# Kernel tuning notes

Hardware: AMD Instinct MI355X
Metric: run time of the kernel (lower is better)

## Reference

```python
import jax, jax.numpy as jnp
import numpy as np

KAPPA = 20.0
STAGES = 10
NUM_PRO = 3
EPS = 1e-6


def _l2norm(x, axis):
    return x / (EPS + jnp.linalg.norm(x, axis=axis, keepdims=True))


def _em(x, mu):
    # x: [b, c, n]; mu: [b, c, k]
    def step(mu, _):
        z = jax.nn.softmax(KAPPA * jnp.einsum('bcn,bck->bnk', x, mu), axis=2)  # [b,n,k]
        z_ = z / (EPS + z.sum(axis=1, keepdims=True))
        mu = _l2norm(jnp.einsum('bcn,bnk->bck', x, z_), axis=1)
        return mu, None
    mu, _ = jax.lax.scan(step, mu, None, length=STAGES)
    return jnp.transpose(mu, (0, 2, 1))  # [b, k, c]


def setup_inputs() -> dict:
    key = jax.random.key(0)
    k1, k2, k3, k4 = jax.random.split(key, 4)
    b, c, h, w, k = 16, 512, 64, 64, NUM_PRO
    support_feature = jax.random.normal(k1, (b, c, h, w), dtype=jnp.float32)
    support_mask = jax.random.uniform(k2, (b, 1, h, w), dtype=jnp.float32)
    query_feature = jax.random.normal(k3, (b, c, h, w), dtype=jnp.float32)
    mu = jax.random.normal(k4, (1, c, k), dtype=jnp.float32) * np.sqrt(2.0 / k)
    return {"support_feature": support_feature, "support_mask": support_mask,
            "query_feature": query_feature, "mu": mu}


def reference(support_feature, support_mask, query_feature, mu):
    b, c, h, w = support_feature.shape
    n = h * w
    mu0 = jnp.broadcast_to(_l2norm(mu, axis=1), (b, c, NUM_PRO))
    # mask already at feature resolution -> bilinear align_corners resize is identity
    z_fg = (support_mask * support_feature).reshape(b, c, n)
    z_bg = ((1.0 - support_mask) * support_feature).reshape(b, c, n)
    mu_f = _em(z_fg, mu0)  # [b, k, c]
    mu_b = _em(z_bg, mu0)  # [b, k, c]
    # discriminative model on query
    mu_cat = jnp.concatenate([mu_f, mu_b], axis=1)  # [b, 2k, c]
    xq = query_feature.reshape(b, c, n)
    z = jax.nn.softmax(jnp.einsum('bcn,bkc->bnk', xq, mu_cat), axis=2)  # [b, n, 2k]
    P = jnp.transpose(z, (0, 2, 1)).reshape(b, 2 * NUM_PRO, h, w)
    P_f = P[:, :NUM_PRO].sum(axis=1, keepdims=True)
    P_b = P[:, NUM_PRO:].sum(axis=1, keepdims=True)
    Prob_map = jnp.concatenate([P_b, P_f], axis=1)  # [b, 2, h, w]
    return (mu_f, mu_b, Prob_map, P)
```

## Files before the change

kernel.cpp:

```cpp
#include <hip/hip_runtime.h>
#include <cstdint>
#include <cstddef>

#define EPS 1e-6f
#define KAPPA 20.0f

#define B 16
#define C 512
#define N 4096
#define J 6
#define XS_STRIDE 513

__global__ __launch_bounds__(512) void pmms_init(const float* __restrict__ mu_in,
                                                 float* __restrict__ mu_cur,
                                                 float* __restrict__ mu_acc) {
  int b = blockIdx.x;
  int c = threadIdx.x;
  float v0 = mu_in[c * 3 + 0], v1 = mu_in[c * 3 + 1], v2 = mu_in[c * 3 + 2];
  float s0 = v0 * v0, s1 = v1 * v1, s2 = v2 * v2;
  for (int o = 32; o; o >>= 1) {
    s0 += __shfl_down(s0, o);
    s1 += __shfl_down(s1, o);
    s2 += __shfl_down(s2, o);
  }
  __shared__ float r[8][3];
  int w = c >> 6, ln = c & 63;
  if (ln == 0) { r[w][0] = s0; r[w][1] = s1; r[w][2] = s2; }
  __syncthreads();
  float t0 = 0.f, t1 = 0.f, t2 = 0.f;
  for (int i = 0; i < 8; ++i) { t0 += r[i][0]; t1 += r[i][1]; t2 += r[i][2]; }
  float sc0 = 1.0f / (EPS + sqrtf(t0));
  float sc1 = 1.0f / (EPS + sqrtf(t1));
  float sc2 = 1.0f / (EPS + sqrtf(t2));
  float n0 = v0 * sc0, n1 = v1 * sc1, n2 = v2 * sc2;
  size_t base = ((size_t)b * C + c) * J;
  mu_cur[base + 0] = n0; mu_cur[base + 1] = n1; mu_cur[base + 2] = n2;
  mu_cur[base + 3] = n0; mu_cur[base + 4] = n1; mu_cur[base + 5] = n2;
  #pragma unroll
  for (int j = 0; j < J; ++j) mu_acc[base + j] = 0.0f;
}

__global__ __launch_bounds__(256, 1) void pmms_stage(const float* __restrict__ feat,
                                                     const float* __restrict__ mask,
                                                     const float* __restrict__ mu_cur,
                                                     float* __restrict__ mu_acc) {
  extern __shared__ float s[];
  float* xs  = s;
  float* mus = xs + 64 * XS_STRIDE;
  float* ms  = mus + C * 8;
  float* zs  = ms + 64;
  float* ps  = zs + 64 * 8;

  int b  = blockIdx.x >> 4;
  int wg = blockIdx.x & 15;
  int tid = threadIdx.x;

  for (int i = tid; i < C * J; i += 256) {
    int c = i / 6, j = i - c * 6;
    mus[c * 8 + j] = mu_cur[(size_t)b * C * J + i];
  }

  float acc[12];
  #pragma unroll
  for (int j = 0; j < 12; ++j) acc[j] = 0.0f;

  const int wv = tid >> 6, ln = tid & 63;

  for (int t = 0; t < 4; ++t) {
    int n0 = (wg * 4 + t) * 64;
    __syncthreads();
    {
      int rpt = tid >> 4, seg = tid & 15;
      const float* fb = feat + (size_t)b * C * N + n0;
      for (int cb = 0; cb < C; cb += 16) {
        int c = cb + rpt;
        float4 v = *(const float4*)(fb + (size_t)c * N + seg * 4);
        int nl = seg * 4;
        xs[(nl + 0) * XS_STRIDE + c] = v.x;
        xs[(nl + 1) * XS_STRIDE + c] = v.y;
        xs[(nl + 2) * XS_STRIDE + c] = v.z;
        xs[(nl + 3) * XS_STRIDE + c] = v.w;
      }
      if (tid < 16) {
        float4 v = *(const float4*)(mask + (size_t)b * N + n0 + tid * 4);
        ms[tid * 4 + 0] = v.x; ms[tid * 4 + 1] = v.y;
        ms[tid * 4 + 2] = v.z; ms[tid * 4 + 3] = v.w;
      }
    }
    __syncthreads();
    {
      float m = ms[ln];
      float lf0 = 0.f, lf1 = 0.f, lf2 = 0.f, lb0 = 0.f, lb1 = 0.f, lb2 = 0.f;
      int cbeg = wv * 128;
      #pragma unroll 4
      for (int c = cbeg; c < cbeg + 128; ++c) {
        float f = xs[ln * XS_STRIDE + c];
        float xf = m * f, xb = f - xf;
        float4 m03 = *(const float4*)(mus + c * 8);
        float2 m45 = *(const float2*)(mus + c * 8 + 4);
        lf0 = fmaf(xf, m03.x, lf0); lf1 = fmaf(xf, m03.y, lf1); lf2 = fmaf(xf, m03.z, lf2);
        lb0 = fmaf(xb, m03.w, lb0); lb1 = fmaf(xb, m45.x, lb1); lb2 = fmaf(xb, m45.y, lb2);
      }
      float* pr = ps + (wv * 64 + ln) * 8;
      pr[0] = lf0; pr[1] = lf1; pr[2] = lf2; pr[3] = lb0; pr[4] = lb1; pr[5] = lb2;
    }
    __syncthreads();
    if (tid < 64) {
      float L[6];
      #pragma unroll
      for (int j = 0; j < 6; ++j)
        L[j] = ps[(0 * 64 + tid) * 8 + j] + ps[(1 * 64 + tid) * 8 + j] +
               ps[(2 * 64 + tid) * 8 + j] + ps[(3 * 64 + tid) * 8 + j];
      float mf = fmaxf(fmaxf(L[0], L[1]), L[2]);
      float e0 = __expf(KAPPA * (L[0] - mf));
      float e1 = __expf(KAPPA * (L[1] - mf));
      float e2 = __expf(KAPPA * (L[2] - mf));
      float is = 1.0f / (e0 + e1 + e2);
      zs[tid * 8 + 0] = e0 * is; zs[tid * 8 + 1] = e1 * is; zs[tid * 8 + 2] = e2 * is;
      float mb = fmaxf(fmaxf(L[3], L[4]), L[5]);
      e0 = __expf(KAPPA * (L[3] - mb));
      e1 = __expf(KAPPA * (L[4] - mb));
      e2 = __expf(KAPPA * (L[5] - mb));
      is = 1.0f / (e0 + e1 + e2);
      zs[tid * 8 + 3] = e0 * is; zs[tid * 8 + 4] = e1 * is; zs[tid * 8 + 5] = e2 * is;
    }
    __syncthreads();
    {
      int c0 = tid, c1 = tid + 256;
      #pragma unroll 4
      for (int n = 0; n < 64; ++n) {
        float m2 = ms[n];
        float4 z03 = *(const float4*)(zs + n * 8);
        float2 z45 = *(const float2*)(zs + n * 8 + 4);
        float f0 = xs[n * XS_STRIDE + c0];
        float xf = m2 * f0, xb = f0 - xf;
        acc[0] = fmaf(xf, z03.x, acc[0]); acc[1] = fmaf(xf, z03.y, acc[1]); acc[2] = fmaf(xf, z03.z, acc[2]);
        acc[3] = fmaf(xb, z03.w, acc[3]); acc[4] = fmaf(xb, z45.x, acc[4]); acc[5] = fmaf(xb, z45.y, acc[5]);
        float f1 = xs[n * XS_STRIDE + c1];
        xf = m2 * f1; xb = f1 - xf;
        acc[6] = fmaf(xf, z03.x, acc[6]); acc[7]  = fmaf(xf, z03.y, acc[7]);  acc[8]  = fmaf(xf, z03.z, acc[8]);
        acc[9] = fmaf(xb, z03.w, acc[9]); acc[10] = fmaf(xb, z45.x, acc[10]); acc[11] = fmaf(xb, z45.y, acc[11]);
      }
    }
  }
  float* dst = mu_acc + (size_t)b * C * J;
  #pragma unroll
  for (int j = 0; j < 6; ++j) atomicAdd(dst + tid * 6 + j, acc[j]);
  #pragma unroll
  for (int j = 0; j < 6; ++j) atomicAdd(dst + (size_t)(tid + 256) * 6 + j, acc[6 + j]);
}

__global__ __launch_bounds__(256) void pmms_norm(float* __restrict__ mu_acc,
                                                 float* __restrict__ mu_cur,
                                                 float* __restrict__ out_f,
                                                 float* __restrict__ out_b,
                                                 int write_out) {
  int b = blockIdx.x / 6, j = blockIdx.x % 6;
  int tid = threadIdx.x;
  size_t base = (size_t)b * C * J + j;
  float v0 = mu_acc[base + (size_t)tid * 6];
  float v1 = mu_acc[base + (size_t)(tid + 256) * 6];
  float ss = v0 * v0 + v1 * v1;
  for (int o = 32; o; o >>= 1) ss += __shfl_down(ss, o);
  __shared__ float r[4];
  if ((tid & 63) == 0) r[tid >> 6] = ss;
  __syncthreads();
  float tot = r[0] + r[1] + r[2] + r[3];
  float sc = 1.0f / (EPS + sqrtf(tot));
  float n0 = v0 * sc, n1 = v1 * sc;
  mu_cur[base + (size_t)tid * 6] = n0;
  mu_cur[base + (size_t)(tid + 256) * 6] = n1;
  mu_acc[base + (size_t)tid * 6] = 0.0f;
  mu_acc[base + (size_t)(tid + 256) * 6] = 0.0f;
  if (write_out) {
    float* o = (j < 3) ? (out_f + (size_t)b * 1536 + j * 512)
                       : (out_b + (size_t)b * 1536 + (j - 3) * 512);
    o[tid] = n0;
    o[tid + 256] = n1;
  }
}

__global__ __launch_bounds__(256) void pmms_query(const float* __restrict__ q,
                                                  const float* __restrict__ mu_cur,
                                                  float* __restrict__ P,
                                                  float* __restrict__ PM) {
  __shared__ float mus[C * 8];
  int b = blockIdx.x >> 4;
  int n = ((blockIdx.x & 15) << 8) + threadIdx.x;
  for (int i = threadIdx.x; i < C * J; i += 256) {
    int c = i / 6, j = i - c * 6;
    mus[c * 8 + j] = mu_cur[(size_t)b * C * J + i];
  }
  __syncthreads();
  float l0 = 0.f, l1 = 0.f, l2 = 0.f, l3 = 0.f, l4 = 0.f, l5 = 0.f;
  const float* qb = q + (size_t)b * C * N + n;
  #pragma unroll 4
  for (int c = 0; c < C; ++c) {
    float xv = qb[(size_t)c * N];
    float4 m03 = *(const float4*)(mus + c * 8);
    float2 m45 = *(const float2*)(mus + c * 8 + 4);
    l0 = fmaf(xv, m03.x, l0); l1 = fmaf(xv, m03.y, l1); l2 = fmaf(xv, m03.z, l2);
    l3 = fmaf(xv, m03.w, l3); l4 = fmaf(xv, m45.x, l4); l5 = fmaf(xv, m45.y, l5);
  }
  float mx = fmaxf(fmaxf(fmaxf(l0, l1), fmaxf(l2, l3)), fmaxf(l4, l5));
  float e0 = __expf(l0 - mx), e1 = __expf(l1 - mx), e2 = __expf(l2 - mx);
  float e3 = __expf(l3 - mx), e4 = __expf(l4 - mx), e5 = __expf(l5 - mx);
  float is = 1.0f / (e0 + e1 + e2 + e3 + e4 + e5);
  float z0 = e0 * is, z1 = e1 * is, z2 = e2 * is;
  float z3 = e3 * is, z4 = e4 * is, z5 = e5 * is;
  float* Pb = P + (size_t)b * 6 * N;
  Pb[0 * N + n] = z0; Pb[1 * N + n] = z1; Pb[2 * N + n] = z2;
  Pb[3 * N + n] = z3; Pb[4 * N + n] = z4; Pb[5 * N + n] = z5;
  float* pm = PM + (size_t)b * 2 * N;
  pm[n] = z3 + z4 + z5;
  pm[N + n] = z0 + z1 + z2;
}

extern "C" void kernel_launch(void* const* d_in, const int* in_sizes, int n_in,
                              void* d_out, int out_size, void* d_ws, size_t ws_size,
                              hipStream_t stream) {
  const float* feat  = (const float*)d_in[0];
  const float* mask  = (const float*)d_in[1];
  const float* query = (const float*)d_in[2];
  const float* mu_in = (const float*)d_in[3];
  float* out = (float*)d_out;

  float* mu_cur = (float*)d_ws;
  float* mu_acc = mu_cur + (size_t)B * C * J;

  const int smem = (64 * XS_STRIDE + C * 8 + 64 + 64 * 8 + 4 * 64 * 8) * 4;
  (void)hipFuncSetAttribute((const void*)pmms_stage,
                            hipFuncAttributeMaxDynamicSharedMemorySize, smem);

  pmms_init<<<B, 512, 0, stream>>>(mu_in, mu_cur, mu_acc);
  for (int st = 0; st < 10; ++st) {
    pmms_stage<<<256, 256, smem, stream>>>(feat, mask, mu_cur, mu_acc);
    pmms_norm<<<96, 256, 0, stream>>>(mu_acc, mu_cur, out, out + 24576, st == 9 ? 1 : 0);
  }
  pmms_query<<<256, 256, 0, stream>>>(query, mu_cur, out + 180224, out + 49152);
}
```

Baseline: 943.2 us.

## Drop shared-memory feature transpose; stream features twice from global with smaller tiles

The stage kernel no longer stages a 64x512 transposed feature tile in LDS. It computes logits straight from global float4 loads, using 8-lane channel splits reduced with shuffles. The weighted sum then rereads the same 128-column tile from global, hoping for L2 hits. Cutting LDS use from about 150KB to about 19KB lets up to 6 blocks share a CU, and the grid grows to 512 blocks. The query kernel uses the same vectorised, shuffle-reduced layout with float4 output stores. The risk is that every stage now reads the features from global twice.

Measured after the change: 1.431 ms. 1.52x slower.

```diff
diff --git a/kernel.cpp b/kernel.cpp
--- a/kernel.cpp
+++ b/kernel.cpp
@@ -9,7 +9,8 @@
 #define C 512
 #define N 4096
 #define J 6
-#define XS_STRIDE 513
+#define NT 128
+#define NTILES (N / NT)
 
 __global__ __launch_bounds__(512) void pmms_init(const float* __restrict__ mu_in,
                                                  float* __restrict__ mu_cur,
@@ -40,106 +41,128 @@
   for (int j = 0; j < J; ++j) mu_acc[base + j] = 0.0f;
 }
 
-__global__ __launch_bounds__(256, 1) void pmms_stage(const float* __restrict__ feat,
+__global__ __launch_bounds__(256, 6) void pmms_stage(const float* __restrict__ feat,
                                                      const float* __restrict__ mask,
                                                      const float* __restrict__ mu_cur,
                                                      float* __restrict__ mu_acc) {
-  extern __shared__ float s[];
-  float* xs  = s;
-  float* mus = xs + 64 * XS_STRIDE;
-  float* ms  = mus + C * 8;
-  float* zs  = ms + 64;
-  float* ps  = zs + 64 * 8;
-
-  int b  = blockIdx.x >> 4;
-  int wg = blockIdx.x & 15;
-  int tid = threadIdx.x;
+  __shared__ float mus[C * 8];
+  __shared__ float zs[J][NT];
+  __shared__ float ms[NT];
+
+  const int b  = blockIdx.x >> 5;
+  const int n0 = (blockIdx.x & 31) * NT;
+  const int tid = threadIdx.x;
 
   for (int i = tid; i < C * J; i += 256) {
     int c = i / 6, j = i - c * 6;
     mus[c * 8 + j] = mu_cur[(size_t)b * C * J + i];
   }
+  if (tid < NT / 4) {
+    *(float4*)(ms + tid * 4) = *(const float4*)(mask + (size_t)b * N + n0 + tid * 4);
+  }
+  __syncthreads();
+
+  {
+    const int cc = tid & 7, ng = tid >> 3;
+    const int nb = n0 + ng * 4;
+    float4 m4 = *(const float4*)(ms + ng * 4);
+    float L[J][4];
+    #pragma unroll
+    for (int j = 0; j < J; ++j)
+      #pragma unroll
+      for (int k = 0; k < 4; ++k) L[j][k] = 0.0f;
+    const float* fb = feat + (size_t)b * C * N + nb;
+    #pragma unroll 4
+    for (int i = 0; i < C / 8; ++i) {
+      int c = cc + i * 8;
+      float4 f   = *(const float4*)(fb + (size_t)c * N);
+      float4 m03 = *(const float4*)(mus + c * 8);
+      float2 m45 = *(const float2*)(mus + c * 8 + 4);
+      float fa[4] = {f.x, f.y, f.z, f.w};
+      float ma[4] = {m4.x, m4.y, m4.z, m4.w};
+      #pragma unroll
+      for (int k = 0; k < 4; ++k) {
+        float xf = ma[k] * fa[k];
+        float xb = fa[k] - xf;
+        L[0][k] = fmaf(xf, m03.x, L[0][k]);
+        L[1][k] = fmaf(xf, m03.y, L[1][k]);
+        L[2][k] = fmaf(xf, m03.z, L[2][k]);
+        L[3][k] = fmaf(xb, m03.w, L[3][k]);
+        L[4][k] = fmaf(xb, m45.x, L[4][k]);
+        L[5][k] = fmaf(xb, m45.y, L[5][k]);
+      }
+    }
+    #pragma unroll
+    for (int d = 1; d < 8; d <<= 1)
+      #pragma unroll
+      for (int j = 0; j < J; ++j)
+        #pragma unroll
+        for (int k = 0; k < 4; ++k)
+          L[j][k] += __shfl_xor(L[j][k], d);
+    float zv[J][4];
+    #pragma unroll
+    for (int k = 0; k < 4; ++k) {
+      float mf = fmaxf(fmaxf(L[0][k], L[1][k]), L[2][k]);
+      float e0 = __expf(KAPPA * (L[0][k] - mf));
+      float e1 = __expf(KAPPA * (L[1][k] - mf));
+      float e2 = __expf(KAPPA * (L[2][k] - mf));
+      float is = 1.0f / (e0 + e1 + e2);
+      zv[0][k] = e0 * is; zv[1][k] = e1 * is; zv[2][k] = e2 * is;
+      float mb = fmaxf(fmaxf(L[3][k], L[4][k]), L[5][k]);
+      e0 = __expf(KAPPA * (L[3][k] - mb));
+      e1 = __expf(KAPPA * (L[4][k] - mb));
+      e2 = __expf(KAPPA * (L[5][k] - mb));
+      is = 1.0f / (e0 + e1 + e2);
+      zv[3][k] = e0 * is; zv[4][k] = e1 * is; zv[5][k] = e2 * is;
+    }
+    if (cc == 0) {
+      int nl = ng * 4;
+      #pragma unroll
+      for (int j = 0; j < J; ++j)
+        *(float4*)(&zs[j][nl]) = make_float4(zv[j][0], zv[j][1], zv[j][2], zv[j][3]);
+    }
+  }
+  __syncthreads();
 
   float acc[12];
   #pragma unroll
   for (int j = 0; j < 12; ++j) acc[j] = 0.0f;
-
-  const int wv = tid >> 6, ln = tid & 63;
-
-  for (int t = 0; t < 4; ++t) {
-    int n0 = (wg * 4 + t) * 64;
-    __syncthreads();
-    {
-      int rpt = tid >> 4, seg = tid & 15;
-      const float* fb = feat + (size_t)b * C * N + n0;
-      for (int cb = 0; cb < C; cb += 16) {
-        int c = cb + rpt;
-        float4 v = *(const float4*)(fb + (size_t)c * N + seg * 4);
-        int nl = seg * 4;
-        xs[(nl + 0) * XS_STRIDE + c] = v.x;
-        xs[(nl + 1) * XS_STRIDE + c] = v.y;
-        xs[(nl + 2) * XS_STRIDE + c] = v.z;
-        xs[(nl + 3) * XS_STRIDE + c] = v.w;
-      }
-      if (tid < 16) {
-        float4 v = *(const float4*)(mask + (size_t)b * N + n0 + tid * 4);
-        ms[tid * 4 + 0] = v.x; ms[tid * 4 + 1] = v.y;
-        ms[tid * 4 + 2] = v.z; ms[tid * 4 + 3] = v.w;
-      }
-    }
-    __syncthreads();
-    {
-      float m = ms[ln];
-      float lf0 = 0.f, lf1 = 0.f, lf2 = 0.f, lb0 = 0.f, lb1 = 0.f, lb2 = 0.f;
-      int cbeg = wv * 128;
-      #pragma unroll 4
-      for (int c = cbeg; c < cbeg + 128; ++c) {
-        float f = xs[ln * XS_STRIDE + c];
-        float xf = m * f, xb = f - xf;
-        float4 m03 = *(const float4*)(mus + c * 8);
-        float2 m45 = *(const float2*)(mus + c * 8 + 4);
-        lf0 = fmaf(xf, m03.x, lf0); lf1 = fmaf(xf, m03.y, lf1); lf2 = fmaf(xf, m03.z, lf2);
-        lb0 = fmaf(xb, m03.w, lb0); lb1 = fmaf(xb, m45.x, lb1); lb2 = fmaf(xb, m45.y, lb2);
-      }
-      float* pr = ps + (wv * 64 + ln) * 8;
-      pr[0] = lf0; pr[1] = lf1; pr[2] = lf2; pr[3] = lb0; pr[4] = lb1; pr[5] = lb2;
-    }
-    __syncthreads();
-    if (tid < 64) {
-      float L[6];
-      #pragma unroll
-      for (int j = 0; j < 6; ++j)
-        L[j] = ps[(0 * 64 + tid) * 8 + j] + ps[(1 * 64 + tid) * 8 + j] +
-               ps[(2 * 64 + tid) * 8 + j] + ps[(3 * 64 + tid) * 8 + j];
-      float mf = fmaxf(fmaxf(L[0], L[1]), L[2]);
-      float e0 = __expf(KAPPA * (L[0] - mf));
-      float e1 = __expf(KAPPA * (L[1] - mf));
-      float e2 = __expf(KAPPA * (L[2] - mf));
-      float is = 1.0f / (e0 + e1 + e2);
-      zs[tid * 8 + 0] = e0 * is; zs[tid * 8 + 1] = e1 * is; zs[tid * 8 + 2] = e2 * is;
-      float mb = fmaxf(fmaxf(L[3], L[4]), L[5]);
-      e0 = __expf(KAPPA * (L[3] - mb));
-      e1 = __expf(KAPPA * (L[4] - mb));
-      e2 = __expf(KAPPA * (L[5] - mb));
-      is = 1.0f / (e0 + e1 + e2);
-      zs[tid * 8 + 3] = e0 * is; zs[tid * 8 + 4] = e1 * is; zs[tid * 8 + 5] = e2 * is;
-    }
-    __syncthreads();
-    {
-      int c0 = tid, c1 = tid + 256;
-      #pragma unroll 4
-      for (int n = 0; n < 64; ++n) {
-        float m2 = ms[n];
-        float4 z03 = *(const float4*)(zs + n * 8);
-        float2 z45 = *(const float2*)(zs + n * 8 + 4);
-        float f0 = xs[n * XS_STRIDE + c0];
-        float xf = m2 * f0, xb = f0 - xf;
-        acc[0] = fmaf(xf, z03.x, acc[0]); acc[1] = fmaf(xf, z03.y, acc[1]); acc[2] = fmaf(xf, z03.z, acc[2]);
-        acc[3] = fmaf(xb, z03.w, acc[3]); acc[4] = fmaf(xb, z45.x, acc[4]); acc[5] = fmaf(xb, z45.y, acc[5]);
-        float f1 = xs[n * XS_STRIDE + c1];
-        xf = m2 * f1; xb = f1 - xf;
-        acc[6] = fmaf(xf, z03.x, acc[6]); acc[7]  = fmaf(xf, z03.y, acc[7]);  acc[8]  = fmaf(xf, z03.z, acc[8]);
-        acc[9] = fmaf(xb, z03.w, acc[9]); acc[10] = fmaf(xb, z45.x, acc[10]); acc[11] = fmaf(xb, z45.y, acc[11]);
+  {
+    const int c0 = tid, c1 = tid + 256;
+    const float* f0p = feat + ((size_t)b * C + c0) * N + n0;
+    const float* f1p = feat + ((size_t)b * C + c1) * N + n0;
+    #pragma unroll 2
+    for (int g = 0; g < NT / 4; ++g) {
+      float4 f0 = *(const float4*)(f0p + g * 4);
+      float4 f1 = *(const float4*)(f1p + g * 4);
+      float4 mm = *(const float4*)(ms + g * 4);
+      float4 z0 = *(const float4*)(&zs[0][g * 4]);
+      float4 z1 = *(const float4*)(&zs[1][g * 4]);
+      float4 z2 = *(const float4*)(&zs[2][g * 4]);
+      float4 z3 = *(const float4*)(&zs[3][g * 4]);
+      float4 z4 = *(const float4*)(&zs[4][g * 4]);
+      float4 z5 = *(const float4*)(&zs[5][g * 4]);
+      float fa0[4] = {f0.x, f0.y, f0.z, f0.w};
+      float fa1[4] = {f1.x, f1.y, f1.z, f1.w};
+      float mk[4]  = {mm.x, mm.y, mm.z, mm.w};
+      float za[J][4] = {{z0.x,z0.y,z0.z,z0.w},{z1.x,z1.y,z1.z,z1.w},{z2.x,z2.y,z2.z,z2.w},
+                        {z3.x,z3.y,z3.z,z3.w},{z4.x,z4.y,z4.z,z4.w},{z5.x,z5.y,z5.z,z5.w}};
+      #pragma unroll
+      for (int k = 0; k < 4; ++k) {
+        float xf = mk[k] * fa0[k], xb = fa0[k] - xf;
+        acc[0] = fmaf(xf, za[0][k], acc[0]);
+        acc[1] = fmaf(xf, za[1][k], acc[1]);
+        acc[2] = fmaf(xf, za[2][k], acc[2]);
+        acc[3] = fmaf(xb, za[3][k], acc[3]);
+        acc[4] = fmaf(xb, za[4][k], acc[4]);
+        acc[5] = fmaf(xb, za[5][k], acc[5]);
+        xf = mk[k] * fa1[k]; xb = fa1[k] - xf;
+        acc[6]  = fmaf(xf, za[0][k], acc[6]);
+        acc[7]  = fmaf(xf, za[1][k], acc[7]);
+        acc[8]  = fmaf(xf, za[2][k], acc[8]);
+        acc[9]  = fmaf(xb, za[3][k], acc[9]);
+        acc[10] = fmaf(xb, za[4][k], acc[10]);
+        acc[11] = fmaf(xb, za[5][k], acc[11]);
       }
     }
   }
@@ -180,40 +203,76 @@
   }
 }
 
-__global__ __launch_bounds__(256) void pmms_query(const float* __restrict__ q,
-                                                  const float* __restrict__ mu_cur,
-                                                  float* __restrict__ P,
-                                                  float* __restrict__ PM) {
+__global__ __launch_bounds__(256, 6) void pmms_query(const float* __restrict__ q,
+                                                     const float* __restrict__ mu_cur,
+                                                     float* __restrict__ P,
+                                                     float* __restrict__ PM) {
   __shared__ float mus[C * 8];
-  int b = blockIdx.x >> 4;
-  int n = ((blockIdx.x & 15) << 8) + threadIdx.x;
-  for (int i = threadIdx.x; i < C * J; i += 256) {
+  const int b  = blockIdx.x >> 5;
+  const int n0 = (blockIdx.x & 31) * NT;
+  const int tid = threadIdx.x;
+  for (int i = tid; i < C * J; i += 256) {
     int c = i / 6, j = i - c * 6;
     mus[c * 8 + j] = mu_cur[(size_t)b * C * J + i];
   }
   __syncthreads();
-  float l0 = 0.f, l1 = 0.f, l2 = 0.f, l3 = 0.f, l4 = 0.f, l5 = 0.f;
-  const float* qb = q + (size_t)b * C * N + n;
+  const int cc = tid & 7, ng = tid >> 3;
+  const int nb = n0 + ng * 4;
+  float L[J][4];
+  #pragma unroll
+  for (int j = 0; j < J; ++j)
+    #pragma unroll
+    for (int k = 0; k < 4; ++k) L[j][k] = 0.0f;
+  const float* qb = q + (size_t)b * C * N + nb;
   #pragma unroll 4
-  for (int c = 0; c < C; ++c) {
-    float xv = qb[(size_t)c * N];
+  for (int i = 0; i < C / 8; ++i) {
+    int c = cc + i * 8;
+    float4 f   = *(const float4*)(qb + (size_t)c * N);
     float4 m03 = *(const float4*)(mus + c * 8);
     float2 m45 = *(const float2*)(mus + c * 8 + 4);
-    l0 = fmaf(xv, m03.x, l0); l1 = fmaf(xv, m03.y, l1); l2 = fmaf(xv, m03.z, l2);
-    l3 = fmaf(xv, m03.w, l3); l4 = fmaf(xv, m45.x, l4); l5 = fmaf(xv, m45.y, l5);
-  }
-  float mx = fmaxf(fmaxf(fmaxf(l0, l1), fmaxf(l2, l3)), fmaxf(l4, l5));
-  float e0 = __expf(l0 - mx), e1 = __expf(l1 - mx), e2 = __expf(l2 - mx);
-  float e3 = __expf(l3 - mx), e4 = __expf(l4 - mx), e5 = __expf(l5 - mx);
-  float is = 1.0f / (e0 + e1 + e2 + e3 + e4 + e5);
-  float z0 = e0 * is, z1 = e1 * is, z2 = e2 * is;
-  float z3 = e3 * is, z4 = e4 * is, z5 = e5 * is;
-  float* Pb = P + (size_t)b * 6 * N;
-  Pb[0 * N + n] = z0; Pb[1 * N + n] = z1; Pb[2 * N + n] = z2;
-  Pb[3 * N + n] = z3; Pb[4 * N + n] = z4; Pb[5 * N + n] = z5;
-  float* pm = PM + (size_t)b * 2 * N;
-  pm[n] = z3 + z4 + z5;
-  pm[N + n] = z0 + z1 + z2;
+    float fa[4] = {f.x, f.y, f.z, f.w};
+    #pragma unroll
+    for (int k = 0; k < 4; ++k) {
+      L[0][k] = fmaf(fa[k], m03.x, L[0][k]);
+      L[1][k] = fmaf(fa[k], m03.y, L[1][k]);
+      L[2][k] = fmaf(fa[k], m03.z, L[2][k]);
+      L[3][k] = fmaf(fa[k], m03.w, L[3][k]);
+      L[4][k] = fmaf(fa[k], m45.x, L[4][k]);
+      L[5][k] = fmaf(fa[k], m45.y, L[5][k]);
+    }
+  }
+  #pragma unroll
+  for (int d = 1; d < 8; d <<= 1)
+    #pragma unroll
+    for (int j = 0; j < J; ++j)
+      #pragma unroll
+      for (int k = 0; k < 4; ++k)
+        L[j][k] += __shfl_xor(L[j][k], d);
+  float zv[J][4];
+  #pragma unroll
+  for (int k = 0; k < 4; ++k) {
+    float mx = fmaxf(fmaxf(fmaxf(L[0][k], L[1][k]), fmaxf(L[2][k], L[3][k])), fmaxf(L[4][k], L[5][k]));
+    float e0 = __expf(L[0][k] - mx), e1 = __expf(L[1][k] - mx), e2 = __expf(L[2][k] - mx);
+    float e3 = __expf(L[3][k] - mx), e4 = __expf(L[4][k] - mx), e5 = __expf(L[5][k] - mx);
+    float is = 1.0f / (e0 + e1 + e2 + e3 + e4 + e5);
+    zv[0][k] = e0 * is; zv[1][k] = e1 * is; zv[2][k] = e2 * is;
+    zv[3][k] = e3 * is; zv[4][k] = e4 * is; zv[5][k] = e5 * is;
+  }
+  if (cc == 0) {
+    float* Pb = P + (size_t)b * 6 * N;
+    #pragma unroll
+    for (int j = 0; j < J; ++j)
+      *(float4*)(Pb + (size_t)j * N + nb) = make_float4(zv[j][0], zv[j][1], zv[j][2], zv[j][3]);
+    float* pm = PM + (size_t)b * 2 * N;
+    *(float4*)(pm + nb) = make_float4(zv[3][0] + zv[4][0] + zv[5][0],
+                                      zv[3][1] + zv[4][1] + zv[5][1],
+                                      zv[3][2] + zv[4][2] + zv[5][2],
+                                      zv[3][3] + zv[4][3] + zv[5][3]);
+    *(float4*)(pm + N + nb) = make_float4(zv[0][0] + zv[1][0] + zv[2][0],
+                                          zv[0][1] + zv[1][1] + zv[2][1],
+                                          zv[0][2] + zv[1][2] + zv[2][2],
+                                          zv[0][3] + zv[1][3] + zv[2][3]);
+  }
 }
 
 extern "C" void kernel_launch(void* const* d_in, const int* in_sizes, int n_in,
@@ -228,14 +287,10 @@
   float* mu_cur = (float*)d_ws;
   float* mu_acc = mu_cur + (size_t)B * C * J;
 
-  const int smem = (64 * XS_STRIDE + C * 8 + 64 + 64 * 8 + 4 * 64 * 8) * 4;
-  (void)hipFuncSetAttribute((const void*)pmms_stage,
-                            hipFuncAttributeMaxDynamicSharedMemorySize, smem);
-
   pmms_init<<<B, 512, 0, stream>>>(mu_in, mu_cur, mu_acc);
   for (int st = 0; st < 10; ++st) {
-    pmms_stage<<<256, 256, smem, stream>>>(feat, mask, mu_cur, mu_acc);
+    pmms_stage<<<B * NTILES, 256, 0, stream>>>(feat, mask, mu_cur, mu_acc);
     pmms_norm<<<96, 256, 0, stream>>>(mu_acc, mu_cur, out, out + 24576, st == 9 ? 1 : 0);
   }
-  pmms_query<<<256, 256, 0, stream>>>(query, mu_cur, out + 180224, out + 49152);
-}
+  pmms_query<<<B * NTILES, 256, 0, stream>>>(query, mu_cur, out + 180224, out + 49152);
+}
```
